# Optimization experiments

Measured on AMD Instinct MI355X. Metric: run time of the kernel, lower is better.

## Reference

```python
import jax, jax.numpy as jnp
import numpy as np

B, L, C, H = 4, 2048, 1024, 16
D = C // H
MAX_SCALE_MUL = float(np.log(100.0))
EPS = 1e-12


def setup_inputs() -> dict:
    key = jax.random.key(0)
    ks = jax.random.split(key, 7)
    return {
        "x": jax.random.normal(ks[0], (B, L, C), dtype=jnp.float32),
        "W_qkv": jax.random.normal(ks[1], (3 * C, C), dtype=jnp.float32) * (C ** -0.5),
        "q_bias": jax.random.normal(ks[2], (C,), dtype=jnp.float32) * 0.02,
        "v_bias": jax.random.normal(ks[3], (C,), dtype=jnp.float32) * 0.02,
        "scale_mul_log": jnp.full((1, H, 1, 1), np.log(4.0), dtype=jnp.float32),
        "W_proj": jax.random.normal(ks[4], (C, C), dtype=jnp.float32) * (C ** -0.5),
        "b_proj": jax.random.normal(ks[5], (C,), dtype=jnp.float32) * 0.02,
    }


def reference(x, W_qkv, q_bias, v_bias, scale_mul_log, W_proj, b_proj):
    Bb, Ll, Cc = x.shape
    # fused QKV projection with bias = cat(q_bias, zeros, v_bias)
    bias = jnp.concatenate([q_bias, jnp.zeros_like(q_bias), v_bias])
    qkv = (x @ W_qkv.T + bias).reshape(Bb, Ll, 3, H, D)
    q, k, v = (jnp.transpose(qkv[:, :, i], (0, 2, 1, 3)) for i in range(3))  # [B,H,L,D]
    # L2-norm attention: normalize q,k; learned per-head scale on q (clamped)
    scale_mul = jnp.exp(jnp.minimum(scale_mul_log, MAX_SCALE_MUL))  # [1,H,1,1]
    q = q / jnp.maximum(jnp.linalg.norm(q, axis=-1, keepdims=True), EPS) * scale_mul
    k = k / jnp.maximum(jnp.linalg.norm(k, axis=-1, keepdims=True), EPS)
    # SDPA with scale=1 (attn_l2_norm path), no mask, no dropout (eval)
    scores = jnp.einsum("bhqd,bhkd->bhqk", q, k)
    attn = jax.nn.softmax(scores, axis=-1)
    out = jnp.einsum("bhqk,bhkd->bhqd", attn, v)
    out = jnp.transpose(out, (0, 2, 1, 3)).reshape(Bb, Ll, Cc)
    return out @ W_proj.T + b_proj
```

## Files before the change

kernel.cpp:

```cpp
#include <hip/hip_runtime.h>
#include <hip/hip_bf16.h>


typedef __attribute__((ext_vector_type(8))) short bf16x8;
typedef __attribute__((ext_vector_type(16))) float f32x16;

#define MAXLOG 4.60517018598809f
#define LOG2E  1.4426950408889634f

__device__ __forceinline__ float bf2f(unsigned short u) {
    union { unsigned int i; float f; } v; v.i = ((unsigned int)u) << 16; return v.f;
}
__device__ __forceinline__ unsigned short f2bf(float f) {
    union { float f; unsigned int i; } v; v.f = f;
    unsigned int x = v.i;
    return (unsigned short)((x + 0x7FFFu + ((x >> 16) & 1u)) >> 16);
}
__device__ __forceinline__ unsigned fbits(float f) {
    union { float f; unsigned u; } v; v.f = f; return v.u;
}
__device__ __forceinline__ bf16x8 pack8(const float* __restrict__ p) {
    float4 a = *(const float4*)p;
    float4 b = *(const float4*)(p + 4);
    bf16x8 r;
    r[0] = (short)f2bf(a.x); r[1] = (short)f2bf(a.y);
    r[2] = (short)f2bf(a.z); r[3] = (short)f2bf(a.w);
    r[4] = (short)f2bf(b.x); r[5] = (short)f2bf(b.y);
    r[6] = (short)f2bf(b.z); r[7] = (short)f2bf(b.w);
    return r;
}
__device__ __forceinline__ void gload_lds16(const void* g, void* l) {
    __builtin_amdgcn_global_load_lds((const __attribute__((address_space(1))) void*)g,
                                     (__attribute__((address_space(3))) void*)l, 16, 0, 0);
}

__global__ __launch_bounds__(256) void k_prep(
    const float* __restrict__ x, const float* __restrict__ Wqkv,
    const float* __restrict__ Wp, const float* __restrict__ qbia,
    const float* __restrict__ vbia,
    unsigned short* __restrict__ xb, unsigned short* __restrict__ Wqkvb,
    unsigned short* __restrict__ Wpb, float* __restrict__ bias3)
{
    int i = blockIdx.x * 256 + threadIdx.x;
    if (i < 1048576) {
        *(bf16x8*)&xb[(long)i * 8] = pack8(&x[(long)i * 8]);
    } else if (i < 1441792) {
        int j = i - 1048576;
        *(bf16x8*)&Wqkvb[(long)j * 8] = pack8(&Wqkv[(long)j * 8]);
    } else if (i < 1572864) {
        int j = i - 1441792;
        *(bf16x8*)&Wpb[(long)j * 8] = pack8(&Wp[(long)j * 8]);
    } else if (i < 1573248) {
        int j = (i - 1572864) * 8;
        for (int u = 0; u < 8; ++u) {
            int n = j + u;
            float v = 0.0f;
            if (n < 1024) v = qbia[n];
            else if (n >= 2048) v = vbia[n - 2048];
            bias3[n] = v;
        }
    }
}

template<bool OUT_F32>
__global__ __launch_bounds__(256) void k_gemm_lds(
    const unsigned short* __restrict__ A, const unsigned short* __restrict__ Bh,
    const float* __restrict__ bias, void* __restrict__ Cp, int N, int K)
{
    __shared__ unsigned short As[128 * 32];
    __shared__ unsigned short Bs[128 * 32];
    const int t = threadIdx.x, wave = t >> 6, lane = t & 63;
    const int m32 = lane & 31, half = lane >> 5;
    const int bm = blockIdx.x * 128, bn = blockIdx.y * 128;
    const int wr = (wave >> 1) * 64, wc = (wave & 1) * 64;
    f32x16 acc[2][2] = {};

    const int srow = lane >> 2;
    const int scol = (lane & 3) * 8;
    const int c0 = wave * 2, c1 = wave * 2 + 1;
    const long ga0 = (long)(bm + c0 * 16 + srow) * K + scol;
    const long ga1 = (long)(bm + c1 * 16 + srow) * K + scol;
    const long gb0 = (long)(bn + c0 * 16 + srow) * K + scol;
    const long gb1 = (long)(bn + c1 * 16 + srow) * K + scol;

    for (int kt = 0; kt < K; kt += 32) {
        __syncthreads();
        gload_lds16(&A[ga0 + kt], &As[c0 * 512]);
        gload_lds16(&A[ga1 + kt], &As[c1 * 512]);
        gload_lds16(&Bh[gb0 + kt], &Bs[c0 * 512]);
        gload_lds16(&Bh[gb1 + kt], &Bs[c1 * 512]);
        __syncthreads();
        bf16x8 af[2][2], bfr[2][2];
        for (int mt = 0; mt < 2; ++mt)
            for (int f = 0; f < 2; ++f)
                af[mt][f] = *(const bf16x8*)&As[(wr + mt * 32 + m32) * 32 + f * 16 + half * 8];
        for (int nt = 0; nt < 2; ++nt)
            for (int f = 0; f < 2; ++f)
                bfr[nt][f] = *(const bf16x8*)&Bs[(wc + nt * 32 + m32) * 32 + f * 16 + half * 8];
        for (int f = 0; f < 2; ++f)
            for (int mt = 0; mt < 2; ++mt)
                for (int nt = 0; nt < 2; ++nt)
                    acc[mt][nt] = __builtin_amdgcn_mfma_f32_32x32x16_bf16(
                        af[mt][f], bfr[nt][f], acc[mt][nt], 0, 0, 0);
    }
    for (int mt = 0; mt < 2; ++mt)
        for (int nt = 0; nt < 2; ++nt) {
            int gn = bn + wc + nt * 32 + m32;
            float bv = bias[gn];
            for (int r = 0; r < 16; ++r) {
                int gm = bm + wr + mt * 32 + (r & 3) + 8 * (r >> 2) + 4 * half;
                float val = acc[mt][nt][r] + bv;
                if (OUT_F32) ((float*)Cp)[(long)gm * N + gn] = val;
                else ((unsigned short*)Cp)[(long)gm * N + gn] = f2bf(val);
            }
        }
}

__global__ __launch_bounds__(256) void k_prep_kv(
    const unsigned short* __restrict__ qkv, unsigned short* __restrict__ kb,
    unsigned short* __restrict__ vT)
{
    __shared__ unsigned short Vsh[64 * 72];
    const int t = threadIdx.x;
    const int bh = blockIdx.y, l0 = blockIdx.x * 64;
    const int h = bh & 15, b = bh >> 4;
    const int ll = t >> 2, c16 = (t & 3) * 16;
    const long rowbase = (long)(b * 2048 + l0 + ll) * 3072;

    {
        bf16x8 k0 = *(const bf16x8*)&qkv[rowbase + 1024 + h * 64 + c16];
        bf16x8 k1 = *(const bf16x8*)&qkv[rowbase + 1024 + h * 64 + c16 + 8];
        float e[16]; float ss = 0.f;
        for (int j = 0; j < 8; ++j) { e[j]     = bf2f((unsigned short)k0[j]); ss += e[j] * e[j]; }
        for (int j = 0; j < 8; ++j) { e[8 + j] = bf2f((unsigned short)k1[j]); ss += e[8 + j] * e[8 + j]; }
        ss += __shfl_xor(ss, 1, 64);
        ss += __shfl_xor(ss, 2, 64);
        float rs = 1.0f / fmaxf(sqrtf(ss), 1e-12f);
        bf16x8 o0, o1;
        for (int j = 0; j < 8; ++j) o0[j] = (short)f2bf(e[j] * rs);
        for (int j = 0; j < 8; ++j) o1[j] = (short)f2bf(e[8 + j] * rs);
        long dst = ((long)bh * 2048 + l0 + ll) * 64 + c16;
        *(bf16x8*)&kb[dst]     = o0;
        *(bf16x8*)&kb[dst + 8] = o1;
    }
    *(bf16x8*)&Vsh[ll * 72 + c16]     = *(const bf16x8*)&qkv[rowbase + 2048 + h * 64 + c16];
    *(bf16x8*)&Vsh[ll * 72 + c16 + 8] = *(const bf16x8*)&qkv[rowbase + 2048 + h * 64 + c16 + 8];
    __syncthreads();
    const int d = t >> 2, ls = (t & 3) * 16;
    unsigned short tmp[16];
    for (int j = 0; j < 16; ++j) tmp[j] = Vsh[(ls + j) * 72 + d];
    long dst = (long)(bh * 64 + d) * 2048 + l0 + ls;
    *(bf16x8*)&vT[dst]     = *(bf16x8*)&tmp[0];
    *(bf16x8*)&vT[dst + 8] = *(bf16x8*)&tmp[8];
}

__global__ __launch_bounds__(256, 4) void k_attn32(
    const unsigned short* __restrict__ qkv, const unsigned short* __restrict__ kb,
    const unsigned short* __restrict__ vT, const float* __restrict__ sml,
    unsigned short* __restrict__ attn)
{
    __shared__ unsigned short Ks[2][64 * 72];
    __shared__ unsigned short Vs[2][64 * 72];
    const int t = threadIdx.x, wave = t >> 6, lane = t & 63;
    const int m32 = lane & 31, half = lane >> 5;
    const int wg = blockIdx.x;
    const int logical = (wg & 7) * 128 + (wg >> 3);
    const int bh = logical >> 4, qblk = logical & 15;
    const int h = bh & 15, b = bh >> 4;
    const int q0 = qblk * 128 + wave * 32;
    const float scale = __expf(fminf(sml[h], MAXLOG));
    const float c2 = scale * LOG2E;

    const int qd = m32 >> 2, lo = qd & 3;
    const int prow = ((((lo == 1) || (lo == 2)) ? (qd ^ 3) : qd) << 2) | (m32 & 3);

    bf16x8 aq[4];
    {
        long base = (long)(b * 2048 + q0 + m32) * 3072 + h * 64;
        float e[32]; float ss = 0.f;
        for (int f = 0; f < 4; ++f) {
            aq[f] = *(const bf16x8*)&qkv[base + f * 16 + half * 8];
            for (int j = 0; j < 8; ++j) { float x = bf2f((unsigned short)aq[f][j]); e[f * 8 + j] = x; ss += x * x; }
        }
        ss += __shfl_xor(ss, 32, 64);
        float rs = (scale * LOG2E) / fmaxf(sqrtf(ss), 1e-12f);
        for (int f = 0; f < 4; ++f)
            for (int j = 0; j < 8; ++j) aq[f][j] = (short)f2bf(e[f * 8 + j] * rs);
    }

    f32x16 o0 = {}, o1 = {}, lacc = {};
    bf16x8 ones; for (int i = 0; i < 8; ++i) ones[i] = (short)0x3F80;
    const int sr = t >> 2, sc = (t & 3) * 16;
    const long kbase = (long)bh * 2048 * 64;
    const long vbase = (long)bh * 64 * 2048;

#define LOADT(kt) \
    kpA = *(const bf16x8*)&kb[kbase + (long)((kt) + sr) * 64 + sc];      \
    kpB = *(const bf16x8*)&kb[kbase + (long)((kt) + sr) * 64 + sc + 8];  \
    vpA = *(const bf16x8*)&vT[vbase + (long)sr * 2048 + (kt) + sc];      \
    vpB = *(const bf16x8*)&vT[vbase + (long)sr * 2048 + (kt) + sc + 8];

#define STORET(buf) \
    *(bf16x8*)&Ks[buf][sr * 72 + sc]     = kpA;  \
    *(bf16x8*)&Ks[buf][sr * 72 + sc + 8] = kpB;  \
    *(bf16x8*)&Vs[buf][sr * 72 + sc]     = vpA;  \
    *(bf16x8*)&Vs[buf][sr * 72 + sc + 8] = vpB;

#define ATTN_STEP(KS, VS, SUB) \
    for (int ktile = 0; ktile < 2; ++ktile) {                                              \
        const unsigned short* krow = &KS[(ktile * 32 + prow) * 72 + half * 8];             \
        f32x16 s = {};                                                                     \
        s = __builtin_amdgcn_mfma_f32_32x32x16_bf16(*(const bf16x8*)&krow[0],  aq[0], s, 0, 0, 0); \
        s = __builtin_amdgcn_mfma_f32_32x32x16_bf16(*(const bf16x8*)&krow[16], aq[1], s, 0, 0, 0); \
        s = __builtin_amdgcn_mfma_f32_32x32x16_bf16(*(const bf16x8*)&krow[32], aq[2], s, 0, 0, 0); \
        s = __builtin_amdgcn_mfma_f32_32x32x16_bf16(*(const bf16x8*)&krow[48], aq[3], s, 0, 0, 0); \
        unsigned pu[16];                                                                   \
        for (int j = 0; j < 16; ++j)                                                       \
            pu[j] = fbits(__builtin_amdgcn_exp2f(s[j] - (SUB)));                           \
        uint4 a0u, a1u;                                                                    \
        a0u.x = __builtin_amdgcn_perm(pu[1],  pu[0],  0x07060302u);                        \
        a0u.y = __builtin_amdgcn_perm(pu[3],  pu[2],  0x07060302u);                        \
        a0u.z = __builtin_amdgcn_perm(pu[5],  pu[4],  0x07060302u);                        \
        a0u.w = __builtin_amdgcn_perm(pu[7],  pu[6],  0x07060302u);                        \
        a1u.x = __builtin_amdgcn_perm(pu[9],  pu[8],  0x07060302u);                        \
        a1u.y = __builtin_amdgcn_perm(pu[11], pu[10], 0x07060302u);                        \
        a1u.z = __builtin_amdgcn_perm(pu[13], pu[12], 0x07060302u);                        \
        a1u.w = __builtin_amdgcn_perm(pu[15], pu[14], 0x07060302u);                        \
        bf16x8 ap0, ap1;                                                                   \
        __builtin_memcpy(&ap0, &a0u, 16); __builtin_memcpy(&ap1, &a1u, 16);                \
        for (int c = 0; c < 2; ++c) {                                                      \
            bf16x8 apc = c ? ap1 : ap0;                                                    \
            bf16x8 bv0 = *(const bf16x8*)&VS[m32 * 72        + ktile * 32 + c * 16 + half * 8]; \
            bf16x8 bv1 = *(const bf16x8*)&VS[(32 + m32) * 72 + ktile * 32 + c * 16 + half * 8]; \
            o0   = __builtin_amdgcn_mfma_f32_32x32x16_bf16(apc, bv0, o0, 0, 0, 0);         \
            o1   = __builtin_amdgcn_mfma_f32_32x32x16_bf16(apc, bv1, o1, 0, 0, 0);         \
            lacc = __builtin_amdgcn_mfma_f32_32x32x16_bf16(apc, ones, lacc, 0, 0, 0);      \
        }                                                                                  \
    }

#define KLOOP(SUB) \
    for (int kt = 0; kt < 2048; kt += 128) {                 \
        LOADT(kt + 64)                                       \
        ATTN_STEP(Ks[0], Vs[0], SUB)                         \
        STORET(1)                                            \
        __syncthreads();                                     \
        const bool more = (kt + 128) < 2048;                 \
        if (more) { LOADT(kt + 128) }                        \
        ATTN_STEP(Ks[1], Vs[1], SUB)                         \
        if (more) {                                          \
            STORET(0)                                        \
            __syncthreads();                                 \
        }                                                    \
    }

    bf16x8 kpA, kpB, vpA, vpB;
    LOADT(0)
    STORET(0)
    __syncthreads();

    if (c2 < 30.0f) {
        KLOOP(0.0f)
    } else {
        KLOOP(c2)
    }
#undef LOADT
#undef STORET
#undef ATTN_STEP
#undef KLOOP

    for (int r = 0; r < 16; ++r) {
        int m = (r & 3) + 8 * (r >> 2) + 4 * half;
        float inv = 1.0f / lacc[r];
        long dst = (long)(b * 2048 + q0 + m) * 1024 + h * 64;
        attn[dst + m32]      = f2bf(o0[r] * inv);
        attn[dst + 32 + m32] = f2bf(o1[r] * inv);
    }
}

extern "C" void kernel_launch(void* const* d_in, const int* in_sizes, int n_in,
                              void* d_out, int out_size, void* d_ws, size_t ws_size,
                              hipStream_t stream) {
    const float* x    = (const float*)d_in[0];
    const float* Wqkv = (const float*)d_in[1];
    const float* qbia = (const float*)d_in[2];
    const float* vbia = (const float*)d_in[3];
    const float* sml  = (const float*)d_in[4];
    const float* Wp   = (const float*)d_in[5];
    const float* bp   = (const float*)d_in[6];

    char* ws = (char*)d_ws;
    unsigned short* qkv   = (unsigned short*)ws;
    unsigned short* kbuf  = (unsigned short*)(ws + 50331648);
    unsigned short* Wqkvb = kbuf;
    unsigned short* vT    = (unsigned short*)(ws + 67108864);
    unsigned short* xb    = vT;
    unsigned short* attnb = (unsigned short*)(ws + 83886080);
    float*          bias3 = (float*)(ws + 100663296);
    unsigned short* Wpb   = (unsigned short*)(ws + 100679680);
    float*          out   = (float*)d_out;

    hipLaunchKernelGGL(k_prep, dim3(6146), dim3(256), 0, stream,
                       x, Wqkv, Wp, qbia, vbia, xb, Wqkvb, Wpb, bias3);
    hipLaunchKernelGGL((k_gemm_lds<false>), dim3(64, 24), dim3(256), 0, stream,
                       xb, Wqkvb, bias3, (void*)qkv, 3072, 1024);
    hipLaunchKernelGGL(k_prep_kv, dim3(32, 64), dim3(256), 0, stream, qkv, kbuf, vT);
    hipLaunchKernelGGL(k_attn32, dim3(1024), dim3(256), 0, stream, qkv, kbuf, vT, sml, attnb);
    hipLaunchKernelGGL((k_gemm_lds<true>), dim3(64, 8), dim3(256), 0, stream,
                       attnb, Wpb, bp, (void*)out, 1024, 1024);
}
```

Measured before the change: 292.5 us.

## Load K operands directly from global into registers, dropping K shared-memory staging

The attention kernel no longer stages K tiles in LDS. Each lane loads its MFMA A-operand fragments for K straight from global memory into registers, double-buffered in two register sets and prefetched one 32-key half-tile ahead. This halves LDS use and removes the LDS writes and reads for K. In exchange, every wave in the workgroup fetches the same K rows from global/L2 (four times the traffic versus shared staging), register pressure goes up, and global-load latency is exposed with only a shallow prefetch.

```diff
diff --git a/kernel.cpp b/kernel.cpp
--- a/kernel.cpp
+++ b/kernel.cpp
@@ -159,7 +159,6 @@
     const unsigned short* __restrict__ vT, const float* __restrict__ sml,
     unsigned short* __restrict__ attn)
 {
-    __shared__ unsigned short Ks[2][64 * 72];
     __shared__ unsigned short Vs[2][64 * 72];
     const int t = threadIdx.x, wave = t >> 6, lane = t & 63;
     const int m32 = lane & 31, half = lane >> 5;
@@ -193,27 +192,29 @@
     const int sr = t >> 2, sc = (t & 3) * 16;
     const long kbase = (long)bh * 2048 * 64;
     const long vbase = (long)bh * 64 * 2048;
-
-#define LOADT(kt) \
-    kpA = *(const bf16x8*)&kb[kbase + (long)((kt) + sr) * 64 + sc];      \
-    kpB = *(const bf16x8*)&kb[kbase + (long)((kt) + sr) * 64 + sc + 8];  \
+    const long kbR = kbase + (long)prow * 64 + half * 8;
+
+#define LOADK4(P0, P1, P2, P3, BKT) \
+    P0 = *(const bf16x8*)&kb[kbR + (long)(BKT) * 64];      \
+    P1 = *(const bf16x8*)&kb[kbR + (long)(BKT) * 64 + 16]; \
+    P2 = *(const bf16x8*)&kb[kbR + (long)(BKT) * 64 + 32]; \
+    P3 = *(const bf16x8*)&kb[kbR + (long)(BKT) * 64 + 48];
+
+#define LOADTV(kt) \
     vpA = *(const bf16x8*)&vT[vbase + (long)sr * 2048 + (kt) + sc];      \
     vpB = *(const bf16x8*)&vT[vbase + (long)sr * 2048 + (kt) + sc + 8];
 
-#define STORET(buf) \
-    *(bf16x8*)&Ks[buf][sr * 72 + sc]     = kpA;  \
-    *(bf16x8*)&Ks[buf][sr * 72 + sc + 8] = kpB;  \
+#define STORETV(buf) \
     *(bf16x8*)&Vs[buf][sr * 72 + sc]     = vpA;  \
     *(bf16x8*)&Vs[buf][sr * 72 + sc + 8] = vpB;
 
-#define ATTN_STEP(KS, VS, SUB) \
-    for (int ktile = 0; ktile < 2; ++ktile) {                                              \
-        const unsigned short* krow = &KS[(ktile * 32 + prow) * 72 + half * 8];             \
+#define ATTN_HALF(VS, KTOFF, K0, K1, K2, K3, SUB) \
+    {                                                                                      \
         f32x16 s = {};                                                                     \
-        s = __builtin_amdgcn_mfma_f32_32x32x16_bf16(*(const bf16x8*)&krow[0],  aq[0], s, 0, 0, 0); \
-        s = __builtin_amdgcn_mfma_f32_32x32x16_bf16(*(const bf16x8*)&krow[16], aq[1], s, 0, 0, 0); \
-        s = __builtin_amdgcn_mfma_f32_32x32x16_bf16(*(const bf16x8*)&krow[32], aq[2], s, 0, 0, 0); \
-        s = __builtin_amdgcn_mfma_f32_32x32x16_bf16(*(const bf16x8*)&krow[48], aq[3], s, 0, 0, 0); \
+        s = __builtin_amdgcn_mfma_f32_32x32x16_bf16(K0, aq[0], s, 0, 0, 0);                \
+        s = __builtin_amdgcn_mfma_f32_32x32x16_bf16(K1, aq[1], s, 0, 0, 0);                \
+        s = __builtin_amdgcn_mfma_f32_32x32x16_bf16(K2, aq[2], s, 0, 0, 0);                \
+        s = __builtin_amdgcn_mfma_f32_32x32x16_bf16(K3, aq[3], s, 0, 0, 0);                \
         unsigned pu[16];                                                                   \
         for (int j = 0; j < 16; ++j)                                                       \
             pu[j] = fbits(__builtin_amdgcn_exp2f(s[j] - (SUB)));                           \
@@ -230,8 +231,8 @@
         __builtin_memcpy(&ap0, &a0u, 16); __builtin_memcpy(&ap1, &a1u, 16);                \
         for (int c = 0; c < 2; ++c) {                                                      \
             bf16x8 apc = c ? ap1 : ap0;                                                    \
-            bf16x8 bv0 = *(const bf16x8*)&VS[m32 * 72        + ktile * 32 + c * 16 + half * 8]; \
-            bf16x8 bv1 = *(const bf16x8*)&VS[(32 + m32) * 72 + ktile * 32 + c * 16 + half * 8]; \
+            bf16x8 bv0 = *(const bf16x8*)&VS[m32 * 72        + (KTOFF) + c * 16 + half * 8]; \
+            bf16x8 bv1 = *(const bf16x8*)&VS[(32 + m32) * 72 + (KTOFF) + c * 16 + half * 8]; \
             o0   = __builtin_amdgcn_mfma_f32_32x32x16_bf16(apc, bv0, o0, 0, 0, 0);         \
             o1   = __builtin_amdgcn_mfma_f32_32x32x16_bf16(apc, bv1, o1, 0, 0, 0);         \
             lacc = __builtin_amdgcn_mfma_f32_32x32x16_bf16(apc, ones, lacc, 0, 0, 0);      \
@@ -239,23 +240,32 @@
     }
 
 #define KLOOP(SUB) \
-    for (int kt = 0; kt < 2048; kt += 128) {                 \
-        LOADT(kt + 64)                                       \
-        ATTN_STEP(Ks[0], Vs[0], SUB)                         \
-        STORET(1)                                            \
-        __syncthreads();                                     \
-        const bool more = (kt + 128) < 2048;                 \
-        if (more) { LOADT(kt + 128) }                        \
-        ATTN_STEP(Ks[1], Vs[1], SUB)                         \
-        if (more) {                                          \
-            STORET(0)                                        \
-            __syncthreads();                                 \
-        }                                                    \
-    }
-
-    bf16x8 kpA, kpB, vpA, vpB;
-    LOADT(0)
-    STORET(0)
+    for (int kt = 0; kt < 2048; kt += 128) {                       \
+        LOADTV(kt + 64)                                            \
+        LOADK4(kB0, kB1, kB2, kB3, kt + 32)                        \
+        ATTN_HALF(Vs[0], 0,  kA0, kA1, kA2, kA3, SUB)              \
+        LOADK4(kA0, kA1, kA2, kA3, kt + 64)                        \
+        ATTN_HALF(Vs[0], 32, kB0, kB1, kB2, kB3, SUB)              \
+        STORETV(1)                                                 \
+        __syncthreads();                                           \
+        const bool more = (kt + 128) < 2048;                       \
+        if (more) { LOADTV(kt + 128) }                             \
+        LOADK4(kB0, kB1, kB2, kB3, kt + 96)                        \
+        ATTN_HALF(Vs[1], 0,  kA0, kA1, kA2, kA3, SUB)              \
+        { const int pk = more ? kt + 128 : 0;                      \
+          LOADK4(kA0, kA1, kA2, kA3, pk) }                         \
+        ATTN_HALF(Vs[1], 32, kB0, kB1, kB2, kB3, SUB)              \
+        if (more) {                                                \
+            STORETV(0)                                             \
+            __syncthreads();                                       \
+        }                                                          \
+    }
+
+    bf16x8 kA0, kA1, kA2, kA3, kB0, kB1, kB2, kB3;
+    bf16x8 vpA, vpB;
+    LOADTV(0)
+    LOADK4(kA0, kA1, kA2, kA3, 0)
+    STORETV(0)
     __syncthreads();
 
     if (c2 < 30.0f) {
@@ -263,9 +273,10 @@
     } else {
         KLOOP(c2)
     }
-#undef LOADT
-#undef STORET
-#undef ATTN_STEP
+#undef LOADK4
+#undef LOADTV
+#undef STORETV
+#undef ATTN_HALF
 #undef KLOOP
 
     for (int r = 0; r < 16; ++r) {
```

Measured after the change: 334.7 us. +14.4%, slower.

## Process two 32-row query tiles per wave in attention to reuse K/V fragments

Applied to the files above, without the earlier changes.

Each wave in the attention kernel now handles 64 query rows (two 32-row MFMA tiles) instead of 32, so every K fragment and V fragment loaded from LDS feeds two sets of MFMAs. Workgroups cover 256 queries, the grid is halved to 512 blocks, and launch bounds drop to 2 blocks per SM to allow the larger register footprint. This cuts LDS traffic and K/V global loads per query, at the cost of fewer resident waves and fewer workgroups to spread across the CUs.

```diff
diff --git a/kernel.cpp b/kernel.cpp
--- a/kernel.cpp
+++ b/kernel.cpp
@@ -154,7 +154,7 @@
     *(bf16x8*)&vT[dst + 8] = *(bf16x8*)&tmp[8];
 }
 
-__global__ __launch_bounds__(256, 4) void k_attn32(
+__global__ __launch_bounds__(256, 2) void k_attn32(
     const unsigned short* __restrict__ qkv, const unsigned short* __restrict__ kb,
     const unsigned short* __restrict__ vT, const float* __restrict__ sml,
     unsigned short* __restrict__ attn)
@@ -164,31 +164,44 @@
     const int t = threadIdx.x, wave = t >> 6, lane = t & 63;
     const int m32 = lane & 31, half = lane >> 5;
     const int wg = blockIdx.x;
-    const int logical = (wg & 7) * 128 + (wg >> 3);
-    const int bh = logical >> 4, qblk = logical & 15;
+    const int logical = (wg & 7) * 64 + (wg >> 3);
+    const int bh = logical >> 3, qblk = logical & 7;
     const int h = bh & 15, b = bh >> 4;
-    const int q0 = qblk * 128 + wave * 32;
+    const int q0 = qblk * 256 + wave * 64;
     const float scale = __expf(fminf(sml[h], MAXLOG));
     const float c2 = scale * LOG2E;
 
     const int qd = m32 >> 2, lo = qd & 3;
     const int prow = ((((lo == 1) || (lo == 2)) ? (qd ^ 3) : qd) << 2) | (m32 & 3);
 
-    bf16x8 aq[4];
+    bf16x8 aqA[4], aqB[4];
     {
         long base = (long)(b * 2048 + q0 + m32) * 3072 + h * 64;
         float e[32]; float ss = 0.f;
         for (int f = 0; f < 4; ++f) {
-            aq[f] = *(const bf16x8*)&qkv[base + f * 16 + half * 8];
-            for (int j = 0; j < 8; ++j) { float x = bf2f((unsigned short)aq[f][j]); e[f * 8 + j] = x; ss += x * x; }
+            aqA[f] = *(const bf16x8*)&qkv[base + f * 16 + half * 8];
+            for (int j = 0; j < 8; ++j) { float x = bf2f((unsigned short)aqA[f][j]); e[f * 8 + j] = x; ss += x * x; }
         }
         ss += __shfl_xor(ss, 32, 64);
         float rs = (scale * LOG2E) / fmaxf(sqrtf(ss), 1e-12f);
         for (int f = 0; f < 4; ++f)
-            for (int j = 0; j < 8; ++j) aq[f][j] = (short)f2bf(e[f * 8 + j] * rs);
-    }
-
-    f32x16 o0 = {}, o1 = {}, lacc = {};
+            for (int j = 0; j < 8; ++j) aqA[f][j] = (short)f2bf(e[f * 8 + j] * rs);
+    }
+    {
+        long base = (long)(b * 2048 + q0 + 32 + m32) * 3072 + h * 64;
+        float e[32]; float ss = 0.f;
+        for (int f = 0; f < 4; ++f) {
+            aqB[f] = *(const bf16x8*)&qkv[base + f * 16 + half * 8];
+            for (int j = 0; j < 8; ++j) { float x = bf2f((unsigned short)aqB[f][j]); e[f * 8 + j] = x; ss += x * x; }
+        }
+        ss += __shfl_xor(ss, 32, 64);
+        float rs = (scale * LOG2E) / fmaxf(sqrtf(ss), 1e-12f);
+        for (int f = 0; f < 4; ++f)
+            for (int j = 0; j < 8; ++j) aqB[f][j] = (short)f2bf(e[f * 8 + j] * rs);
+    }
+
+    f32x16 oA0 = {}, oA1 = {}, lA = {};
+    f32x16 oB0 = {}, oB1 = {}, lB = {};
     bf16x8 ones; for (int i = 0; i < 8; ++i) ones[i] = (short)0x3F80;
     const int sr = t >> 2, sc = (t & 3) * 16;
     const long kbase = (long)bh * 2048 * 64;
@@ -206,14 +219,13 @@
     *(bf16x8*)&Vs[buf][sr * 72 + sc]     = vpA;  \
     *(bf16x8*)&Vs[buf][sr * 72 + sc + 8] = vpB;
 
-#define ATTN_STEP(KS, VS, SUB) \
-    for (int ktile = 0; ktile < 2; ++ktile) {                                              \
-        const unsigned short* krow = &KS[(ktile * 32 + prow) * 72 + half * 8];             \
+#define SCORE(AQ, AP0, AP1, KF0, KF1, KF2, KF3, SUB) \
+    {                                                                                      \
         f32x16 s = {};                                                                     \
-        s = __builtin_amdgcn_mfma_f32_32x32x16_bf16(*(const bf16x8*)&krow[0],  aq[0], s, 0, 0, 0); \
-        s = __builtin_amdgcn_mfma_f32_32x32x16_bf16(*(const bf16x8*)&krow[16], aq[1], s, 0, 0, 0); \
-        s = __builtin_amdgcn_mfma_f32_32x32x16_bf16(*(const bf16x8*)&krow[32], aq[2], s, 0, 0, 0); \
-        s = __builtin_amdgcn_mfma_f32_32x32x16_bf16(*(const bf16x8*)&krow[48], aq[3], s, 0, 0, 0); \
+        s = __builtin_amdgcn_mfma_f32_32x32x16_bf16(KF0, AQ[0], s, 0, 0, 0);               \
+        s = __builtin_amdgcn_mfma_f32_32x32x16_bf16(KF1, AQ[1], s, 0, 0, 0);               \
+        s = __builtin_amdgcn_mfma_f32_32x32x16_bf16(KF2, AQ[2], s, 0, 0, 0);               \
+        s = __builtin_amdgcn_mfma_f32_32x32x16_bf16(KF3, AQ[3], s, 0, 0, 0);               \
         unsigned pu[16];                                                                   \
         for (int j = 0; j < 16; ++j)                                                       \
             pu[j] = fbits(__builtin_amdgcn_exp2f(s[j] - (SUB)));                           \
@@ -226,15 +238,30 @@
         a1u.y = __builtin_amdgcn_perm(pu[11], pu[10], 0x07060302u);                        \
         a1u.z = __builtin_amdgcn_perm(pu[13], pu[12], 0x07060302u);                        \
         a1u.w = __builtin_amdgcn_perm(pu[15], pu[14], 0x07060302u);                        \
-        bf16x8 ap0, ap1;                                                                   \
-        __builtin_memcpy(&ap0, &a0u, 16); __builtin_memcpy(&ap1, &a1u, 16);                \
+        __builtin_memcpy(&AP0, &a0u, 16); __builtin_memcpy(&AP1, &a1u, 16);                \
+    }
+
+#define ATTN_STEP(KS, VS, SUB) \
+    for (int ktile = 0; ktile < 2; ++ktile) {                                              \
+        const unsigned short* krow = &KS[(ktile * 32 + prow) * 72 + half * 8];             \
+        bf16x8 kf0 = *(const bf16x8*)&krow[0];                                             \
+        bf16x8 kf1 = *(const bf16x8*)&krow[16];                                            \
+        bf16x8 kf2 = *(const bf16x8*)&krow[32];                                            \
+        bf16x8 kf3 = *(const bf16x8*)&krow[48];                                            \
+        bf16x8 apA0, apA1, apB0, apB1;                                                     \
+        SCORE(aqA, apA0, apA1, kf0, kf1, kf2, kf3, SUB)                                    \
+        SCORE(aqB, apB0, apB1, kf0, kf1, kf2, kf3, SUB)                                    \
         for (int c = 0; c < 2; ++c) {                                                      \
-            bf16x8 apc = c ? ap1 : ap0;                                                    \
+            bf16x8 aA = c ? apA1 : apA0;                                                   \
+            bf16x8 aB = c ? apB1 : apB0;                                                   \
             bf16x8 bv0 = *(const bf16x8*)&VS[m32 * 72        + ktile * 32 + c * 16 + half * 8]; \
             bf16x8 bv1 = *(const bf16x8*)&VS[(32 + m32) * 72 + ktile * 32 + c * 16 + half * 8]; \
-            o0   = __builtin_amdgcn_mfma_f32_32x32x16_bf16(apc, bv0, o0, 0, 0, 0);         \
-            o1   = __builtin_amdgcn_mfma_f32_32x32x16_bf16(apc, bv1, o1, 0, 0, 0);         \
-            lacc = __builtin_amdgcn_mfma_f32_32x32x16_bf16(apc, ones, lacc, 0, 0, 0);      \
+            oA0 = __builtin_amdgcn_mfma_f32_32x32x16_bf16(aA, bv0, oA0, 0, 0, 0);          \
+            oA1 = __builtin_amdgcn_mfma_f32_32x32x16_bf16(aA, bv1, oA1, 0, 0, 0);          \
+            lA  = __builtin_amdgcn_mfma_f32_32x32x16_bf16(aA, ones, lA, 0, 0, 0);          \
+            oB0 = __builtin_amdgcn_mfma_f32_32x32x16_bf16(aB, bv0, oB0, 0, 0, 0);          \
+            oB1 = __builtin_amdgcn_mfma_f32_32x32x16_bf16(aB, bv1, oB1, 0, 0, 0);          \
+            lB  = __builtin_amdgcn_mfma_f32_32x32x16_bf16(aB, ones, lB, 0, 0, 0);          \
         }                                                                                  \
     }
 
@@ -265,15 +292,20 @@
     }
 #undef LOADT
 #undef STORET
+#undef SCORE
 #undef ATTN_STEP
 #undef KLOOP
 
     for (int r = 0; r < 16; ++r) {
         int m = (r & 3) + 8 * (r >> 2) + 4 * half;
-        float inv = 1.0f / lacc[r];
-        long dst = (long)(b * 2048 + q0 + m) * 1024 + h * 64;
-        attn[dst + m32]      = f2bf(o0[r] * inv);
-        attn[dst + 32 + m32] = f2bf(o1[r] * inv);
+        float invA = 1.0f / lA[r];
+        long dstA = (long)(b * 2048 + q0 + m) * 1024 + h * 64;
+        attn[dstA + m32]      = f2bf(oA0[r] * invA);
+        attn[dstA + 32 + m32] = f2bf(oA1[r] * invA);
+        float invB = 1.0f / lB[r];
+        long dstB = (long)(b * 2048 + q0 + 32 + m) * 1024 + h * 64;
+        attn[dstB + m32]      = f2bf(oB0[r] * invB);
+        attn[dstB + 32 + m32] = f2bf(oB1[r] * invB);
     }
 }
 
@@ -304,7 +336,7 @@
     hipLaunchKernelGGL((k_gemm_lds<false>), dim3(64, 24), dim3(256), 0, stream,
                        xb, Wqkvb, bias3, (void*)qkv, 3072, 1024);
     hipLaunchKernelGGL(k_prep_kv, dim3(32, 64), dim3(256), 0, stream, qkv, kbuf, vT);
-    hipLaunchKernelGGL(k_attn32, dim3(1024), dim3(256), 0, stream, qkv, kbuf, vT, sml, attnb);
+    hipLaunchKernelGGL(k_attn32, dim3(512), dim3(256), 0, stream, qkv, kbuf, vT, sml, attnb);
     hipLaunchKernelGGL((k_gemm_lds<true>), dim3(64, 8), dim3(256), 0, stream,
                        attnb, Wpb, bp, (void*)out, 1024, 1024);
 }
```

Measured after the change: 282.5 us. 1.04x faster.
